# Kernel tuning notes

Hardware: AMD Instinct MI355X
Metric: run time of the kernel (lower is better)

Reference implementation:

```python
import jax, jax.numpy as jnp
import numpy as np

R = 0.01          # slice width (init kwarg r)
DIM = 0           # init kwarg dim = 'x'
NUM_SLICES = 101  # static bound: coords ~ U[0,1) so ceil(range/R) <= 100; +1 safety


def setup_inputs() -> dict:
    key = jax.random.key(0)
    k1, k2 = jax.random.split(key)
    B, N = 16, 65536
    x = jax.random.uniform(k1, (B, 3, N), dtype=jnp.float32)      # point coords in [0,1)
    x_64 = jax.random.normal(k2, (B, 64, N), dtype=jnp.float32)   # per-point features
    return {"x": x, "x_64": x_64, "batch_": B, "points": N}


def reference(x, x_64, batch_, points):
    # per-batch min along the chosen axis: [B]
    pmin = x[:, DIM, :].min(axis=1)
    coord = x[:, DIM, :]                                          # [B, N]
    # bucket index per point (torch.floor((point - min)/r))
    k = jnp.floor((coord - pmin[:, None]) / R).astype(jnp.int32)  # [B, N]
    seg = k.reshape(-1)                                           # [B*N] global slice ids (original pools across batch)
    feats = jnp.transpose(x_64, (0, 2, 1)).reshape(-1, 64)        # [B*N, 64]
    # vectorized segment max replacing the python per-slice loop
    max_feature = jax.ops.segment_max(feats, seg, num_segments=NUM_SLICES)  # [NUM_SLICES, 64]
    counts = jax.ops.segment_sum(jnp.ones_like(seg, dtype=jnp.int32), seg,
                                 num_segments=NUM_SLICES)         # [NUM_SLICES] = slice_num
    return max_feature, counts
```

## Files before the change

kernel.cpp:

```cpp
#include <hip/hip_runtime.h>

#define NSEG 101
#define NCH 64
#define NPTS 65536
#define NBATCH 16
#define NMAX (NCH * NSEG)
#define NOUT (NMAX + NSEG)
#define FLT_BIG 3.4028234663852886e38f

#define SENT 0x007FFFFFu
#define BITS_EMPTY 0xFF7F0000u
#define BITS_POS_CLAMP 0x7F7F0000u

static __device__ __forceinline__ unsigned enc(float f) {
    unsigned b = (unsigned)__float_as_int(f);
    return b ^ (0x80000000u | (unsigned)((int)b >> 31));
}
static __device__ __forceinline__ unsigned dec_bits(unsigned u) {
    unsigned flip = (u & 0x80000000u) ? 0x80000000u : 0xFFFFFFFFu;
    return u ^ flip;
}
static __device__ __forceinline__ unsigned finalize_bits(int e, unsigned u) {
    if (e < NMAX) {
        if (u == SENT) return BITS_EMPTY;
        unsigned ob = dec_bits(u);
        unsigned mag = ob & 0x7FFFFFFFu;
        if (mag >= 0x7F7F8000u)
            ob = (ob & 0x80000000u) | BITS_POS_CLAMP;
        return ob;
    }
    return (unsigned)__float_as_int((float)u);
}

__global__ __launch_bounds__(256) void sp6_minp(const float* __restrict__ x,
                                                float* __restrict__ pm_part,
                                                unsigned* __restrict__ acc) {
    int b = blockIdx.x >> 4, ch = blockIdx.x & 15;
    int t = threadIdx.x;

    int e = blockIdx.x * 256 + t;
    if (e < NMAX) acc[e] = SENT;
    else if (e < NOUT) acc[e] = 0u;

    const float4* row = (const float4*)(x + (size_t)b * 3 * NPTS + (size_t)ch * 4096);
    float m = FLT_BIG;
    #pragma unroll
    for (int i = 0; i < 4; i++) {
        float4 v = row[t + i * 256];
        m = fminf(m, fminf(fminf(v.x, v.y), fminf(v.z, v.w)));
    }
    #pragma unroll
    for (int off = 32; off; off >>= 1)
        m = fminf(m, __shfl_down(m, off, 64));
    __shared__ float sm[4];
    if ((t & 63) == 0) sm[t >> 6] = m;
    __syncthreads();
    if (t == 0)
        pm_part[blockIdx.x] = fminf(fminf(sm[0], sm[1]), fminf(sm[2], sm[3]));
}

__global__ void sp6_seed(unsigned* __restrict__ acc) {
    int e = blockIdx.x * 256 + threadIdx.x;
    if (e < NMAX) acc[e] = SENT;
    else if (e < NOUT) acc[e] = 0u;
}

template<bool PMIN_WS>
__global__ __launch_bounds__(512, 4) void sp6_main(const float* __restrict__ x,
                                                   const float* __restrict__ x64,
                                                   const float* __restrict__ pm_part,
                                                   unsigned* __restrict__ acc) {
    __shared__ unsigned smax[NMAX];
    __shared__ unsigned scnt[NSEG];
    int t = threadIdx.x;
    for (int i = t; i < NMAX; i += 512) smax[i] = SENT;
    if (t < NSEG) scnt[t] = 0u;

    int b = blockIdx.x >> 5;
    int chunk = blockIdx.x & 31;

    float pm;
    if constexpr (PMIN_WS) {
        float r = pm_part[b * 16];
        #pragma unroll
        for (int i = 1; i < 16; i++) r = fminf(r, pm_part[b * 16 + i]);
        pm = r;
        __syncthreads();
    } else {
        __shared__ float swmin[8];
        const float4* crow = (const float4*)(x + (size_t)b * 3 * NPTS);
        float m = FLT_BIG;
        #pragma unroll
        for (int i = 0; i < 32; i++) {
            float4 v = crow[t + i * 512];
            m = fminf(m, fminf(fminf(v.x, v.y), fminf(v.z, v.w)));
        }
        #pragma unroll
        for (int off = 32; off; off >>= 1)
            m = fminf(m, __shfl_down(m, off, 64));
        if ((t & 63) == 0) swmin[t >> 6] = m;
        __syncthreads();
        pm = swmin[0];
        #pragma unroll
        for (int i = 1; i < 8; i++) pm = fminf(pm, swmin[i]);
    }

    int n0 = chunk * 2048 + t * 4;
    float4 cv = *(const float4*)(x + (size_t)b * 3 * NPTS + n0);
    int k0 = (int)floorf((cv.x - pm) / 0.01f);
    int k1 = (int)floorf((cv.y - pm) / 0.01f);
    int k2 = (int)floorf((cv.z - pm) / 0.01f);
    int k3 = (int)floorf((cv.w - pm) / 0.01f);
    k0 = k0 < 0 ? 0 : (k0 > NSEG - 1 ? NSEG - 1 : k0);
    k1 = k1 < 0 ? 0 : (k1 > NSEG - 1 ? NSEG - 1 : k1);
    k2 = k2 < 0 ? 0 : (k2 > NSEG - 1 ? NSEG - 1 : k2);
    k3 = k3 < 0 ? 0 : (k3 > NSEG - 1 ? NSEG - 1 : k3);
    atomicAdd(&scnt[k0], 1u);
    atomicAdd(&scnt[k1], 1u);
    atomicAdd(&scnt[k2], 1u);
    atomicAdd(&scnt[k3], 1u);

    const float* gp = x64 + (size_t)b * NCH * NPTS + n0;
    #pragma unroll 8
    for (int c = 0; c < NCH; c++) {
        float4 v = *(const float4*)(gp + (size_t)c * NPTS);
        atomicMax(&smax[c * NSEG + k0], enc(v.x));
        atomicMax(&smax[c * NSEG + k1], enc(v.y));
        atomicMax(&smax[c * NSEG + k2], enc(v.z));
        atomicMax(&smax[c * NSEG + k3], enc(v.w));
    }
    __syncthreads();

    int s = (int)((blockIdx.x * 1283u) % NOUT);
    for (int e = t; e < NOUT; e += 512) {
        int idx = e + s; if (idx >= NOUT) idx -= NOUT;
        if (idx < NMAX) {
            unsigned v = smax[(idx & 63) * NSEG + (idx >> 6)];
            if (v != SENT) atomicMax(&acc[idx], v);
        } else {
            unsigned v = scnt[idx - NMAX];
            if (v) atomicAdd(&acc[idx], v);
        }
    }
}

__global__ void sp6_fin(unsigned* __restrict__ acc) {
    int e = blockIdx.x * 256 + threadIdx.x;
    if (e >= NOUT) return;
    acc[e] = finalize_bits(e, acc[e]);
}

extern "C" void kernel_launch(void* const* d_in, const int* in_sizes, int n_in,
                              void* d_out, int out_size, void* d_ws, size_t ws_size,
                              hipStream_t stream) {
    const float* x   = (const float*)d_in[0];
    const float* x64 = (const float*)d_in[1];
    unsigned* acc = (unsigned*)d_out;
    float* pm_part = (float*)d_ws;

    if (ws_size >= 256 * sizeof(float)) {
        sp6_minp<<<256, 256, 0, stream>>>(x, pm_part, acc);
        sp6_main<true><<<NBATCH * 32, 512, 0, stream>>>(x, x64, pm_part, acc);
    } else {
        sp6_seed<<<(NOUT + 255) / 256, 256, 0, stream>>>(acc);
        sp6_main<false><<<NBATCH * 32, 512, 0, stream>>>(x, x64, nullptr, acc);
    }
    sp6_fin<<<(NOUT + 255) / 256, 256, 0, stream>>>(acc);
}
```

Before: 61.25 us.

## Precompute byte bin indices and run per-channel max with small shared histogram

Adds a binning kernel that computes each point's slice index once, writes it as a byte array to workspace and accumulates the counts. The main kernel now runs one block per (batch, channel) and keeps only a 101-entry shared max table, which cuts LDS use from about 26KB to under 1KB per block and allows higher occupancy. This removes the large shared-memory init and flush of the old design. The cost is an extra launch plus a 1MB byte-index write and re-read, and all 512 threads now contend on a 101-entry array.

```diff
diff --git a/kernel.cpp b/kernel.cpp
--- a/kernel.cpp
+++ b/kernel.cpp
@@ -31,8 +31,12 @@
     }
     return (unsigned)__float_as_int((float)u);
 }
-
-__global__ __launch_bounds__(256) void sp6_minp(const float* __restrict__ x,
+static __device__ __forceinline__ int bink(float c, float pm) {
+    int k = (int)floorf((c - pm) / 0.01f);
+    return k < 0 ? 0 : (k > NSEG - 1 ? NSEG - 1 : k);
+}
+
+__global__ __launch_bounds__(256) void sp7_minp(const float* __restrict__ x,
                                                 float* __restrict__ pm_part,
                                                 unsigned* __restrict__ acc) {
     int b = blockIdx.x >> 4, ch = blockIdx.x & 15;
@@ -59,67 +63,110 @@
         pm_part[blockIdx.x] = fminf(fminf(sm[0], sm[1]), fminf(sm[2], sm[3]));
 }
 
-__global__ void sp6_seed(unsigned* __restrict__ acc) {
+__global__ __launch_bounds__(256) void sp7_bin(const float* __restrict__ x,
+                                               const float* __restrict__ pm_part,
+                                               unsigned char* __restrict__ karr,
+                                               unsigned* __restrict__ acc) {
+    __shared__ unsigned cnt[NSEG];
+    int t = threadIdx.x;
+    if (t < NSEG) cnt[t] = 0u;
+    int b = blockIdx.x >> 4, sub = blockIdx.x & 15;
+
+    float pm = pm_part[b * 16];
+    #pragma unroll
+    for (int i = 1; i < 16; i++) pm = fminf(pm, pm_part[b * 16 + i]);
+    __syncthreads();
+
+    const float* cp = x + (size_t)b * 3 * NPTS + sub * 4096;
+    uchar4* kp = (uchar4*)(karr + (size_t)b * NPTS + sub * 4096);
+    #pragma unroll
+    for (int j = 0; j < 4; j++) {
+        int n4 = j * 256 + t;
+        float4 v = *(const float4*)(cp + n4 * 4);
+        int k0 = bink(v.x, pm), k1 = bink(v.y, pm);
+        int k2 = bink(v.z, pm), k3 = bink(v.w, pm);
+        kp[n4] = make_uchar4((unsigned char)k0, (unsigned char)k1,
+                             (unsigned char)k2, (unsigned char)k3);
+        atomicAdd(&cnt[k0], 1u);
+        atomicAdd(&cnt[k1], 1u);
+        atomicAdd(&cnt[k2], 1u);
+        atomicAdd(&cnt[k3], 1u);
+    }
+    __syncthreads();
+    if (t < NSEG && cnt[t]) atomicAdd(&acc[NMAX + t], cnt[t]);
+}
+
+__global__ __launch_bounds__(512, 8) void sp7_main(const float* __restrict__ x64,
+                                                   const unsigned char* __restrict__ karr,
+                                                   unsigned* __restrict__ acc) {
+    __shared__ unsigned sm[NSEG];
+    int t = threadIdx.x;
+    if (t < NSEG) sm[t] = SENT;
+    int b = blockIdx.x >> 6, c = blockIdx.x & 63;
+    const float4* fp = (const float4*)(x64 + ((size_t)b * NCH + c) * NPTS);
+    const uchar4* kp = (const uchar4*)(karr + (size_t)b * NPTS);
+    __syncthreads();
+
+    #pragma unroll 4
+    for (int j = 0; j < 32; j++) {
+        int n4 = j * 512 + t;
+        float4 v = fp[n4];
+        uchar4 kk = kp[n4];
+        atomicMax(&sm[kk.x], enc(v.x));
+        atomicMax(&sm[kk.y], enc(v.y));
+        atomicMax(&sm[kk.z], enc(v.z));
+        atomicMax(&sm[kk.w], enc(v.w));
+    }
+    __syncthreads();
+
+    if (t < NSEG) {
+        unsigned v = sm[t];
+        if (v != SENT) atomicMax(&acc[t * NCH + c], v);
+    }
+}
+
+__global__ void sp7_fin(unsigned* __restrict__ acc) {
+    int e = blockIdx.x * 256 + threadIdx.x;
+    if (e >= NOUT) return;
+    acc[e] = finalize_bits(e, acc[e]);
+}
+
+__global__ void sp7_seed_fb(unsigned* __restrict__ acc) {
     int e = blockIdx.x * 256 + threadIdx.x;
     if (e < NMAX) acc[e] = SENT;
     else if (e < NOUT) acc[e] = 0u;
 }
-
-template<bool PMIN_WS>
-__global__ __launch_bounds__(512, 4) void sp6_main(const float* __restrict__ x,
-                                                   const float* __restrict__ x64,
-                                                   const float* __restrict__ pm_part,
-                                                   unsigned* __restrict__ acc) {
+__global__ __launch_bounds__(512, 4) void sp7_main_fb(const float* __restrict__ x,
+                                                      const float* __restrict__ x64,
+                                                      unsigned* __restrict__ acc) {
     __shared__ unsigned smax[NMAX];
     __shared__ unsigned scnt[NSEG];
+    __shared__ float swmin[8];
     int t = threadIdx.x;
     for (int i = t; i < NMAX; i += 512) smax[i] = SENT;
     if (t < NSEG) scnt[t] = 0u;
-
-    int b = blockIdx.x >> 5;
-    int chunk = blockIdx.x & 31;
-
-    float pm;
-    if constexpr (PMIN_WS) {
-        float r = pm_part[b * 16];
-        #pragma unroll
-        for (int i = 1; i < 16; i++) r = fminf(r, pm_part[b * 16 + i]);
-        pm = r;
-        __syncthreads();
-    } else {
-        __shared__ float swmin[8];
-        const float4* crow = (const float4*)(x + (size_t)b * 3 * NPTS);
-        float m = FLT_BIG;
-        #pragma unroll
-        for (int i = 0; i < 32; i++) {
-            float4 v = crow[t + i * 512];
-            m = fminf(m, fminf(fminf(v.x, v.y), fminf(v.z, v.w)));
-        }
-        #pragma unroll
-        for (int off = 32; off; off >>= 1)
-            m = fminf(m, __shfl_down(m, off, 64));
-        if ((t & 63) == 0) swmin[t >> 6] = m;
-        __syncthreads();
-        pm = swmin[0];
-        #pragma unroll
-        for (int i = 1; i < 8; i++) pm = fminf(pm, swmin[i]);
-    }
-
+    int b = blockIdx.x >> 5, chunk = blockIdx.x & 31;
+    const float4* crow = (const float4*)(x + (size_t)b * 3 * NPTS);
+    float m = FLT_BIG;
+    #pragma unroll
+    for (int i = 0; i < 32; i++) {
+        float4 v = crow[t + i * 512];
+        m = fminf(m, fminf(fminf(v.x, v.y), fminf(v.z, v.w)));
+    }
+    #pragma unroll
+    for (int off = 32; off; off >>= 1)
+        m = fminf(m, __shfl_down(m, off, 64));
+    if ((t & 63) == 0) swmin[t >> 6] = m;
+    __syncthreads();
+    float pm = swmin[0];
+    #pragma unroll
+    for (int i = 1; i < 8; i++) pm = fminf(pm, swmin[i]);
     int n0 = chunk * 2048 + t * 4;
     float4 cv = *(const float4*)(x + (size_t)b * 3 * NPTS + n0);
-    int k0 = (int)floorf((cv.x - pm) / 0.01f);
-    int k1 = (int)floorf((cv.y - pm) / 0.01f);
-    int k2 = (int)floorf((cv.z - pm) / 0.01f);
-    int k3 = (int)floorf((cv.w - pm) / 0.01f);
-    k0 = k0 < 0 ? 0 : (k0 > NSEG - 1 ? NSEG - 1 : k0);
-    k1 = k1 < 0 ? 0 : (k1 > NSEG - 1 ? NSEG - 1 : k1);
-    k2 = k2 < 0 ? 0 : (k2 > NSEG - 1 ? NSEG - 1 : k2);
-    k3 = k3 < 0 ? 0 : (k3 > NSEG - 1 ? NSEG - 1 : k3);
-    atomicAdd(&scnt[k0], 1u);
-    atomicAdd(&scnt[k1], 1u);
-    atomicAdd(&scnt[k2], 1u);
-    atomicAdd(&scnt[k3], 1u);
-
+    int k0 = bink(cv.x, pm), k1 = bink(cv.y, pm);
+    int k2 = bink(cv.z, pm), k3 = bink(cv.w, pm);
+    atomicAdd(&scnt[k0], 1u); atomicAdd(&scnt[k1], 1u);
+    atomicAdd(&scnt[k2], 1u); atomicAdd(&scnt[k3], 1u);
     const float* gp = x64 + (size_t)b * NCH * NPTS + n0;
     #pragma unroll 8
     for (int c = 0; c < NCH; c++) {
@@ -130,24 +177,15 @@
         atomicMax(&smax[c * NSEG + k3], enc(v.w));
     }
     __syncthreads();
-
-    int s = (int)((blockIdx.x * 1283u) % NOUT);
     for (int e = t; e < NOUT; e += 512) {
-        int idx = e + s; if (idx >= NOUT) idx -= NOUT;
-        if (idx < NMAX) {
-            unsigned v = smax[(idx & 63) * NSEG + (idx >> 6)];
-            if (v != SENT) atomicMax(&acc[idx], v);
+        if (e < NMAX) {
+            unsigned v = smax[(e & 63) * NSEG + (e >> 6)];
+            if (v != SENT) atomicMax(&acc[e], v);
         } else {
-            unsigned v = scnt[idx - NMAX];
-            if (v) atomicAdd(&acc[idx], v);
+            unsigned v = scnt[e - NMAX];
+            if (v) atomicAdd(&acc[e], v);
         }
     }
-}
-
-__global__ void sp6_fin(unsigned* __restrict__ acc) {
-    int e = blockIdx.x * 256 + threadIdx.x;
-    if (e >= NOUT) return;
-    acc[e] = finalize_bits(e, acc[e]);
 }
 
 extern "C" void kernel_launch(void* const* d_in, const int* in_sizes, int n_in,
@@ -157,13 +195,15 @@
     const float* x64 = (const float*)d_in[1];
     unsigned* acc = (unsigned*)d_out;
     float* pm_part = (float*)d_ws;
-
-    if (ws_size >= 256 * sizeof(float)) {
-        sp6_minp<<<256, 256, 0, stream>>>(x, pm_part, acc);
-        sp6_main<true><<<NBATCH * 32, 512, 0, stream>>>(x, x64, pm_part, acc);
+    unsigned char* karr = (unsigned char*)d_ws + 1024;
+
+    if (ws_size >= 1024 + (size_t)NBATCH * NPTS) {
+        sp7_minp<<<256, 256, 0, stream>>>(x, pm_part, acc);
+        sp7_bin<<<256, 256, 0, stream>>>(x, pm_part, karr, acc);
+        sp7_main<<<NBATCH * NCH, 512, 0, stream>>>(x64, karr, acc);
     } else {
-        sp6_seed<<<(NOUT + 255) / 256, 256, 0, stream>>>(acc);
-        sp6_main<false><<<NBATCH * 32, 512, 0, stream>>>(x, x64, nullptr, acc);
-    }
-    sp6_fin<<<(NOUT + 255) / 256, 256, 0, stream>>>(acc);
-}
+        sp7_seed_fb<<<(NOUT + 255) / 256, 256, 0, stream>>>(acc);
+        sp7_main_fb<<<NBATCH * 32, 512, 0, stream>>>(x, x64, acc);
+    }
+    sp7_fin<<<(NOUT + 255) / 256, 256, 0, stream>>>(acc);
+}
```

Measured after the change: 60.93 us. About the same (-0.5%).
